# Kernel optimization log

Hardware: AMD Instinct MI355X
Metric: run time of the kernel (lower is better)

The kernel has to match this reference:

```python
import jax, jax.numpy as jnp
import numpy as np

HID = 51

def _lstm_cell_zero_state(x, w_ih, w_hh, b_ih, b_hh):
    # torch LSTMCell with h=c=0: gates = x @ W_ih^T + b_ih + b_hh (W_hh term vanishes)
    gates = x @ w_ih.T + (b_ih + b_hh)
    i, f, g, o = jnp.split(gates, 4, axis=-1)
    i = jax.nn.sigmoid(i)
    g = jnp.tanh(g)
    o = jax.nn.sigmoid(o)
    c = i * g  # f * c_prev = 0
    h = o * jnp.tanh(c)
    return h


def setup_inputs() -> dict:
    key = jax.random.key(0)
    ks = jax.random.split(key, 12)
    T, B = 200, 2048
    s1 = 1.0  # torch default init is U(-1/sqrt(hid), 1/sqrt(hid))
    bound = 1.0 / np.sqrt(HID)
    u = lambda k, shp: jax.random.uniform(k, shp, jnp.float32, -bound, bound)
    return {
        "x": jax.random.normal(ks[0], (T, B, 1), jnp.float32),
        "w_ih1": u(ks[1], (4 * HID, 1)),
        "w_hh1": u(ks[2], (4 * HID, HID)),
        "b_ih1": u(ks[3], (4 * HID,)),
        "b_hh1": u(ks[4], (4 * HID,)),
        "w_ih2": u(ks[5], (4 * HID, HID)),
        "w_hh2": u(ks[6], (4 * HID, HID)),
        "b_ih2": u(ks[7], (4 * HID,)),
        "b_hh2": u(ks[8], (4 * HID,)),
        "w_lin": u(ks[9], (1, HID)),
        "b_lin": u(ks[10], (1,)),
    }


def reference(x, w_ih1, w_hh1, b_ih1, b_hh1, w_ih2, w_hh2, b_ih2, b_hh2, w_lin, b_lin):
    # Original never carries (h, c) between timesteps -> every timestep is an
    # independent zero-state cell application; vectorize over (T, B) at once.
    T, B, D = x.shape
    xf = x.reshape(T * B, D)
    h1 = _lstm_cell_zero_state(xf, w_ih1, w_hh1, b_ih1, b_hh1)   # [T*B, 51]
    h2 = _lstm_cell_zero_state(h1, w_ih2, w_hh2, b_ih2, b_hh2)   # [T*B, 51]
    out = h2 @ w_lin.T + b_lin                                    # [T*B, 1]
    return out.reshape(T, B, 1)
```

## Files before the change

kernel.cpp:

```cpp
#include <hip/hip_runtime.h>
#include <math.h>


#define NTAB 16384
#define XMIN (-10.0f)
#define XMAX (10.0f)

typedef _Float16 h2_t __attribute__((ext_vector_type(2)));

__device__ __forceinline__ float fexp2_(float x) { return __builtin_amdgcn_exp2f(x); }
__device__ __forceinline__ float frcp_(float x)  { return __builtin_amdgcn_rcpf(x); }
__device__ __forceinline__ float fsig_(float z)  { return frcp_(1.0f + fexp2_(-1.44269504f * z)); }
__device__ __forceinline__ float ftanh_(float z) { return 1.0f - 2.0f * frcp_(1.0f + fexp2_(2.88539008f * z)); }

__global__ __launch_bounds__(256) void repack(
    const float* __restrict__ w_ih2, const float* __restrict__ b_ih2,
    const float* __restrict__ b_hh2, unsigned int* __restrict__ Wp,
    float* __restrict__ B2)
{
    int g = blockIdx.x * 256 + threadIdx.x;
    if (g < 153 * 26) {
        int r = g / 26;
        int p = g - r * 26;
        int src = (r < 51) ? r : r + 51;
        float a = w_ih2[src * 51 + 2 * p];
        float b = (2 * p + 1 < 51) ? w_ih2[src * 51 + 2 * p + 1] : 0.0f;
        h2_t h;
        h.x = (_Float16)a;
        h.y = (_Float16)b;
        Wp[r * 26 + p] = __builtin_bit_cast(unsigned int, h);
    }
    if (g < 153) {
        int src = (g < 51) ? g : g + 51;
        B2[g] = b_ih2[src] + b_hh2[src];
    }
}

__global__ __launch_bounds__(1024, 4) void build_table(
    const float* __restrict__ w_ih1, const float* __restrict__ b_ih1, const float* __restrict__ b_hh1,
    const unsigned int* __restrict__ Wp, const float* __restrict__ B2,
    const float* __restrict__ w_lin, const float* __restrict__ b_lin,
    float* __restrict__ table)
{
    __shared__ float h1s[51][64];
    __shared__ float sPart[16][64];

    const int tid  = threadIdx.x;
    const int lane = tid & 63;
    const int wave = __builtin_amdgcn_readfirstlane(tid >> 6);

    const int   e = blockIdx.x * 64 + lane;
    const float x = XMIN + (XMAX - XMIN) * ((float)e / (float)(NTAB - 1));

    for (int j = wave; j < 51; j += 16) {
        float gi = fmaf(x, w_ih1[j],       b_ih1[j]       + b_hh1[j]);
        float gg = fmaf(x, w_ih1[j + 102], b_ih1[j + 102] + b_hh1[j + 102]);
        float go = fmaf(x, w_ih1[j + 153], b_ih1[j + 153] + b_hh1[j + 153]);
        float c  = fsig_(gi) * ftanh_(gg);
        h1s[j][lane] = fsig_(go) * ftanh_(c);
    }
    __syncthreads();

    h2_t h1p[26];
    #pragma unroll
    for (int p = 0; p < 26; ++p) {
        float a = h1s[2 * p][lane];
        float b = (2 * p + 1 < 51) ? h1s[2 * p + 1][lane] : 0.0f;
        h2_t h;
        h.x = (_Float16)a;
        h.y = (_Float16)b;
        h1p[p] = h;
    }

    float part = 0.0f;
    for (int j = wave; j < 51; j += 16) {
        const unsigned int* __restrict__ Wi = Wp + j * 26;
        const unsigned int* __restrict__ Wg = Wp + (51 + j) * 26;
        const unsigned int* __restrict__ Wo = Wp + (102 + j) * 26;
        float gi = B2[j];
        float gg = B2[51 + j];
        float go = B2[102 + j];
        #pragma unroll
        for (int p = 0; p < 26; ++p) {
            gi = __builtin_amdgcn_fdot2(h1p[p], __builtin_bit_cast(h2_t, Wi[p]), gi, false);
            gg = __builtin_amdgcn_fdot2(h1p[p], __builtin_bit_cast(h2_t, Wg[p]), gg, false);
            go = __builtin_amdgcn_fdot2(h1p[p], __builtin_bit_cast(h2_t, Wo[p]), go, false);
        }
        float c2  = fsig_(gi) * ftanh_(gg);
        float h2v = fsig_(go) * ftanh_(c2);
        part = fmaf(h2v, w_lin[j], part);
    }

    sPart[wave][lane] = part;
    __syncthreads();
    if (wave == 0) {
        float out = b_lin[0];
        #pragma unroll
        for (int w = 0; w < 16; ++w) out += sPart[w][lane];
        table[e] = out;
    }
}

__device__ __forceinline__ float lerp_tab(float x, const float* __restrict__ t) {
    const float inv_h = (float)(NTAB - 1) / (XMAX - XMIN);
    float u = (x - XMIN) * inv_h;
    u = fminf(fmaxf(u, 0.0f), (float)(NTAB - 1) - 0.001f);
    int   i0 = (int)u;
    float f  = u - (float)i0;
    float t0 = t[i0];
    float t1 = t[i0 + 1];
    return fmaf(f, t1 - t0, t0);
}

__global__ __launch_bounds__(256) void lookup_kernel(
    const float* __restrict__ x, const float* __restrict__ table,
    float* __restrict__ out, int n)
{
    int i4 = blockIdx.x * 256 + threadIdx.x;
    int base = i4 * 4;
    if (base + 3 < n) {
        float4 xv = ((const float4*)x)[i4];
        float4 r;
        r.x = lerp_tab(xv.x, table);
        r.y = lerp_tab(xv.y, table);
        r.z = lerp_tab(xv.z, table);
        r.w = lerp_tab(xv.w, table);
        ((float4*)out)[i4] = r;
    } else {
        for (int i = base; i < n; ++i) out[i] = lerp_tab(x[i], table);
    }
}

extern "C" void kernel_launch(void* const* d_in, const int* in_sizes, int n_in,
                              void* d_out, int out_size, void* d_ws, size_t ws_size,
                              hipStream_t stream) {
    const float* x     = (const float*)d_in[0];
    const float* w_ih1 = (const float*)d_in[1];
    const float* b_ih1 = (const float*)d_in[3];
    const float* b_hh1 = (const float*)d_in[4];
    const float* w_ih2 = (const float*)d_in[5];
    const float* b_ih2 = (const float*)d_in[7];
    const float* b_hh2 = (const float*)d_in[8];
    const float* w_lin = (const float*)d_in[9];
    const float* b_lin = (const float*)d_in[10];

    float* out = (float*)d_out;
    float*        table = (float*)d_ws;
    unsigned int* Wp    = (unsigned int*)d_ws + 16384;
    float*        B2    = (float*)d_ws + 16384 + 153 * 26;
    const int n = in_sizes[0];

    repack<<<(153 * 26 + 255) / 256, 256, 0, stream>>>(w_ih2, b_ih2, b_hh2, Wp, B2);

    build_table<<<NTAB / 64, 1024, 0, stream>>>(
        w_ih1, b_ih1, b_hh1, Wp, B2, w_lin, b_lin, table);

    const int n4 = (n + 3) / 4;
    lookup_kernel<<<(n4 + 255) / 256, 256, 0, stream>>>(x, table, out, n);
}
```

Measured before the change: 84.89 us.

## Pack all weights per hidden unit contiguously and double table resolution

Repacks layer-1 weights, layer-2 gate rows, biases and w_lin into one contiguous record per hidden unit so each wave reads a single compact stream. Waves now take contiguous ranges of hidden units instead of striding. The table size doubles to 32768 entries, which doubles build_table work but improves interpolation accuracy. The launch-bounds occupancy hint is raised to 8.

```diff
diff --git a/kernel.cpp b/kernel.cpp
--- a/kernel.cpp
+++ b/kernel.cpp
@@ -2,44 +2,59 @@
 #include <math.h>
 
 
-#define NTAB 16384
+#define NTAB 32768
 #define XMIN (-10.0f)
 #define XMAX (10.0f)
 
+#define W2_STRIDE 84
+#define L1_OFF    (51 * W2_STRIDE)
+#define L1_STRIDE 8
+#define PACK_DWORDS (L1_OFF + 51 * L1_STRIDE)
+
 typedef _Float16 h2_t __attribute__((ext_vector_type(2)));
+
+__device__ __forceinline__ float bcf(unsigned u) { return __builtin_bit_cast(float, u); }
+__device__ __forceinline__ h2_t  bch(unsigned u) { return __builtin_bit_cast(h2_t, u); }
 
 __device__ __forceinline__ float fexp2_(float x) { return __builtin_amdgcn_exp2f(x); }
 __device__ __forceinline__ float frcp_(float x)  { return __builtin_amdgcn_rcpf(x); }
 __device__ __forceinline__ float fsig_(float z)  { return frcp_(1.0f + fexp2_(-1.44269504f * z)); }
 __device__ __forceinline__ float ftanh_(float z) { return 1.0f - 2.0f * frcp_(1.0f + fexp2_(2.88539008f * z)); }
 
-__global__ __launch_bounds__(256) void repack(
-    const float* __restrict__ w_ih2, const float* __restrict__ b_ih2,
-    const float* __restrict__ b_hh2, unsigned int* __restrict__ Wp,
-    float* __restrict__ B2)
+__global__ __launch_bounds__(128) void repack(
+    const float* __restrict__ w_ih1, const float* __restrict__ b_ih1, const float* __restrict__ b_hh1,
+    const float* __restrict__ w_ih2, const float* __restrict__ b_ih2, const float* __restrict__ b_hh2,
+    const float* __restrict__ w_lin, unsigned* __restrict__ P)
 {
-    int g = blockIdx.x * 256 + threadIdx.x;
-    if (g < 153 * 26) {
-        int r = g / 26;
-        int p = g - r * 26;
-        int src = (r < 51) ? r : r + 51;
+    const int j = blockIdx.x;
+    const int t = threadIdx.x;
+    unsigned* R = P + j * W2_STRIDE;
+    if (t < 78) {
+        int g = t / 26, p = t - g * 26;
+        int src = j + (g == 0 ? 0 : (g == 1 ? 102 : 153));
         float a = w_ih2[src * 51 + 2 * p];
         float b = (2 * p + 1 < 51) ? w_ih2[src * 51 + 2 * p + 1] : 0.0f;
         h2_t h;
         h.x = (_Float16)a;
         h.y = (_Float16)b;
-        Wp[r * 26 + p] = __builtin_bit_cast(unsigned int, h);
-    }
-    if (g < 153) {
-        int src = (g < 51) ? g : g + 51;
-        B2[g] = b_ih2[src] + b_hh2[src];
+        R[t] = __builtin_bit_cast(unsigned, h);
+    } else if (t < 81) {
+        int g = t - 78;
+        int src = j + (g == 0 ? 0 : (g == 1 ? 102 : 153));
+        R[t] = __builtin_bit_cast(unsigned, b_ih2[src] + b_hh2[src]);
+    } else if (t == 81) {
+        R[81] = __builtin_bit_cast(unsigned, w_lin[j]);
+    } else if (t >= 88 && t < 94) {
+        int q  = t - 88;
+        int gq = (q < 3) ? q : q - 3;
+        int src = j + (gq == 0 ? 0 : (gq == 1 ? 102 : 153));
+        float v = (q < 3) ? w_ih1[src] : (b_ih1[src] + b_hh1[src]);
+        (P + L1_OFF + j * L1_STRIDE)[q] = __builtin_bit_cast(unsigned, v);
     }
 }
 
-__global__ __launch_bounds__(1024, 4) void build_table(
-    const float* __restrict__ w_ih1, const float* __restrict__ b_ih1, const float* __restrict__ b_hh1,
-    const unsigned int* __restrict__ Wp, const float* __restrict__ B2,
-    const float* __restrict__ w_lin, const float* __restrict__ b_lin,
+__global__ __launch_bounds__(1024, 8) void build_table(
+    const unsigned* __restrict__ P, const float* __restrict__ b_lin,
     float* __restrict__ table)
 {
     __shared__ float h1s[51][64];
@@ -52,10 +67,14 @@
     const int   e = blockIdx.x * 64 + lane;
     const float x = XMIN + (XMAX - XMIN) * ((float)e / (float)(NTAB - 1));
 
-    for (int j = wave; j < 51; j += 16) {
-        float gi = fmaf(x, w_ih1[j],       b_ih1[j]       + b_hh1[j]);
-        float gg = fmaf(x, w_ih1[j + 102], b_ih1[j + 102] + b_hh1[j + 102]);
-        float go = fmaf(x, w_ih1[j + 153], b_ih1[j + 153] + b_hh1[j + 153]);
+    const int j0 = (51 * wave) >> 4;
+    const int j1 = (51 * (wave + 1)) >> 4;
+
+    for (int j = j0; j < j1; ++j) {
+        const unsigned* __restrict__ L = P + L1_OFF + j * L1_STRIDE;
+        float gi = fmaf(x, bcf(L[0]), bcf(L[3]));
+        float gg = fmaf(x, bcf(L[1]), bcf(L[4]));
+        float go = fmaf(x, bcf(L[2]), bcf(L[5]));
         float c  = fsig_(gi) * ftanh_(gg);
         h1s[j][lane] = fsig_(go) * ftanh_(c);
     }
@@ -73,22 +92,20 @@
     }
 
     float part = 0.0f;
-    for (int j = wave; j < 51; j += 16) {
-        const unsigned int* __restrict__ Wi = Wp + j * 26;
-        const unsigned int* __restrict__ Wg = Wp + (51 + j) * 26;
-        const unsigned int* __restrict__ Wo = Wp + (102 + j) * 26;
-        float gi = B2[j];
-        float gg = B2[51 + j];
-        float go = B2[102 + j];
+    for (int j = j0; j < j1; ++j) {
+        const unsigned* __restrict__ R = P + j * W2_STRIDE;
+        float gi = bcf(R[78]);
+        float gg = bcf(R[79]);
+        float go = bcf(R[80]);
         #pragma unroll
         for (int p = 0; p < 26; ++p) {
-            gi = __builtin_amdgcn_fdot2(h1p[p], __builtin_bit_cast(h2_t, Wi[p]), gi, false);
-            gg = __builtin_amdgcn_fdot2(h1p[p], __builtin_bit_cast(h2_t, Wg[p]), gg, false);
-            go = __builtin_amdgcn_fdot2(h1p[p], __builtin_bit_cast(h2_t, Wo[p]), go, false);
+            gi = __builtin_amdgcn_fdot2(h1p[p], bch(R[p]),      gi, false);
+            gg = __builtin_amdgcn_fdot2(h1p[p], bch(R[26 + p]), gg, false);
+            go = __builtin_amdgcn_fdot2(h1p[p], bch(R[52 + p]), go, false);
         }
         float c2  = fsig_(gi) * ftanh_(gg);
         float h2v = fsig_(go) * ftanh_(c2);
-        part = fmaf(h2v, w_lin[j], part);
+        part = fmaf(h2v, bcf(R[81]), part);
     }
 
     sPart[wave][lane] = part;
@@ -145,15 +162,13 @@
     const float* b_lin = (const float*)d_in[10];
 
     float* out = (float*)d_out;
-    float*        table = (float*)d_ws;
-    unsigned int* Wp    = (unsigned int*)d_ws + 16384;
-    float*        B2    = (float*)d_ws + 16384 + 153 * 26;
+    float*    table = (float*)d_ws;
+    unsigned* P     = (unsigned*)d_ws + NTAB;
     const int n = in_sizes[0];
 
-    repack<<<(153 * 26 + 255) / 256, 256, 0, stream>>>(w_ih2, b_ih2, b_hh2, Wp, B2);
+    repack<<<51, 128, 0, stream>>>(w_ih1, b_ih1, b_hh1, w_ih2, b_ih2, b_hh2, w_lin, P);
 
-    build_table<<<NTAB / 64, 1024, 0, stream>>>(
-        w_ih1, b_ih1, b_hh1, Wp, B2, w_lin, b_lin, table);
+    build_table<<<NTAB / 64, 1024, 0, stream>>>(P, b_lin, table);
 
     const int n4 = (n + 3) / 4;
     lookup_kernel<<<(n4 + 255) / 256, 256, 0, stream>>>(x, table, out, n);
```

Result: slower. 87.47 us (+3.0%).
